# Performance work log

Hardware: AMD Instinct MI355X
Metric: run time of the kernel (lower is better)

Reference implementation:

```python
import jax, jax.numpy as jnp
import numpy as np

NC = 5          # tess_size: number of cells on [0,1]
EPS = 1e-10
BIG = 1e10      # stand-in for 'never hits boundary'


def _make_basis(nC):
    # Continuity constraints of the piecewise-affine velocity v(x)=a_c x + b_c
    # at interior knots x_k = k/nC; basis = null space of L via SVD (basis='svd').
    L = np.zeros((nC - 1, 2 * nC), dtype=np.float64)
    for k in range(1, nC):
        xk = k / nC
        i = k - 1
        L[i, 2 * i: 2 * i + 2] = [xk, 1.0]
        L[i, 2 * (i + 1): 2 * (i + 1) + 2] = [-xk, -1.0]
    _, _, Vt = np.linalg.svd(L)
    return np.ascontiguousarray(Vt[nC - 1:].T).astype(np.float32)  # (2nC, nC+1)

_B = _make_basis(NC)


def _cpab_transform(x, A):
    """Closed-form integration of the CPA ODE x' = a_c x + b_c for unit time.
    x: (N,) points in [0,1]; A: (nC,2) per-cell (slope, offset).
    Returns (phi(x), dphi/dx). dphi/dx = exp(sum_c a_c * time_in_cell_c).
    Boundary cells extend to +/- inf (zero_boundary=False)."""
    nC = NC
    t_rem = jnp.ones_like(x)
    logjac = jnp.zeros_like(x)
    done = jnp.zeros(x.shape, dtype=bool)
    for _ in range(nC + 1):  # at most nC-1 cell crossings possible
        c = jnp.clip(jnp.floor(x * nC).astype(jnp.int32), 0, nC - 1)
        ac = A[c, 0]
        bc = A[c, 1]
        v = ac * x + bc
        pos = v >= 0
        xb = jnp.where(pos, c + 1, c).astype(x.dtype) / nC   # target boundary
        at_edge = jnp.where(pos, c == nC - 1, c == 0)        # boundary cell: no exit
        vb = ac * xb + bc
        v_safe = jnp.where(jnp.abs(v) > EPS, v, 1.0)
        a_safe = jnp.where(jnp.abs(ac) > EPS, ac, 1.0)
        ratio = vb / v_safe
        # time to hit boundary: log(v(xb)/v(x))/a  (or linear if a==0)
        t_hit = jnp.where(jnp.abs(ac) > EPS,
                          jnp.log(jnp.where(ratio > EPS, ratio, 1.0)) / a_safe,
                          (xb - x) / v_safe)
        valid = (jnp.abs(v) > EPS) & (ratio > EPS) & (~at_edge)
        t_hit = jnp.where(valid, t_hit, BIG)
        cross = (t_hit < t_rem) & (~done)
        t_step = jnp.where(done, 0.0, jnp.where(cross, t_hit, t_rem))
        # in-cell flow: x + v * expm1(a t)/a  (-> x + v t as a -> 0)
        e = jnp.expm1(ac * t_step)
        x_flow = jnp.where(jnp.abs(ac) > EPS, x + v * e / a_safe, x + v * t_step)
        x = jnp.where(done, x, jnp.where(cross, xb, x_flow))
        logjac = logjac + ac * t_step
        t_rem = t_rem - t_step
        done = done | (~cross)
    return x, jnp.exp(logjac)


def setup_inputs() -> dict:
    key = jax.random.key(0)
    k1, k2 = jax.random.split(key)
    N = 4_194_304
    x = jax.random.uniform(k1, (N,), dtype=jnp.float32)
    theta = jax.random.normal(k2, (NC + 1,), dtype=jnp.float32)
    return {
        "x": x,
        "theta": theta,
        "aff_a": jnp.ones((1,), jnp.float32),
        "aff_b": jnp.zeros((1,), jnp.float32),
        "aff_c": jnp.ones((1,), jnp.float32),
        "aff_d": jnp.zeros((1,), jnp.float32),
    }


def reference(x, theta, aff_a, aff_b, aff_c, aff_d):
    B = jnp.asarray(_B)                      # (2nC, d)
    A = (B @ theta).reshape(NC, 2)           # per-cell (slope, offset)
    y = aff_a * x + aff_b
    w, dw_dy = _cpab_transform(y, A)         # T.transform_grid / T.gradient_space
    z = aff_c * w + aff_d
    dz_dx = aff_c * dw_dy * aff_a
    return z, jnp.log(dz_dx)
```

## Files before the change

kernel.cpp:

```cpp
#include <hip/hip_runtime.h>
#include <math.h>

#define NC 5
#define NBASIS (NC + 1)
#define EPSF 1e-10f
#define BIGF 1e10f

typedef float v4f __attribute__((ext_vector_type(4)));

struct BMat { float b[2 * NC][NBASIS]; };

static BMat compute_basis() {
    const int m = NC - 1;
    const int n = 2 * NC;
    double A[NC - 1][2 * NC];
    for (int r = 0; r < m; ++r)
        for (int c = 0; c < n; ++c) A[r][c] = 0.0;
    for (int k = 1; k < NC; ++k) {
        double xk = (double)k / (double)NC;
        int i = k - 1;
        A[i][2 * i]     = xk;   A[i][2 * i + 1] = 1.0;
        A[i][2 * i + 2] = -xk;  A[i][2 * i + 3] = -1.0;
    }
    double tau[NC - 1];
    for (int i = 0; i < m; ++i) {
        double alpha = A[i][i];
        double xs = 0.0;
        for (int j = i + 1; j < n; ++j) xs += A[i][j] * A[i][j];
        double xnorm = sqrt(xs);
        if (xnorm == 0.0) { tau[i] = 0.0; continue; }
        double beta = (alpha >= 0.0 ? -1.0 : 1.0) * sqrt(alpha * alpha + xs);
        tau[i] = (beta - alpha) / beta;
        double inv = 1.0 / (alpha - beta);
        for (int j = i + 1; j < n; ++j) A[i][j] *= inv;
        A[i][i] = beta;
        for (int r = i + 1; r < m; ++r) {
            double dot = A[r][i];
            for (int j = i + 1; j < n; ++j) dot += A[r][j] * A[i][j];
            dot *= tau[i];
            A[r][i] -= dot;
            for (int j = i + 1; j < n; ++j) A[r][j] -= dot * A[i][j];
        }
    }
    BMat B;
    for (int c = 0; c < NBASIS; ++c) {
        double v[2 * NC];
        for (int r = 0; r < n; ++r) v[r] = 0.0;
        v[m + c] = 1.0;
        for (int i = m - 1; i >= 0; --i) {
            double dot = v[i];
            for (int j = i + 1; j < n; ++j) dot += A[i][j] * v[j];
            dot *= tau[i];
            v[i] -= dot;
            for (int j = i + 1; j < n; ++j) v[j] -= dot * A[i][j];
        }
        for (int r = 0; r < n; ++r) B.b[r][c] = (float)v[r];
    }
    return B;
}

__device__ __forceinline__ void classify_pt(
    float ym, int c, float a, float b, float kL, float kR,
    float vL, float vR, const float* tR, int& kind, int& jf)
{
#pragma clang fp contract(off)
    float v = a * ym + b;
    bool pos = (v >= 0.0f);
    float xb = pos ? kR : kL;
    bool at_edge = pos ? (c == NC - 1) : (c == 0);
    float vb = pos ? vR : vL;
    bool vok = fabsf(v) > EPSF;
    float vs = vok ? v : 1.0f;
    float ratio = vb / vs;
    bool aok = fabsf(a) > EPSF;
    float as = aok ? a : 1.0f;
    float t0 = aok ? (logf(ratio > EPSF ? ratio : 1.0f) / as)
                   : ((xb - ym) / vs);
    bool valid = vok && (ratio > EPSF) && (!at_edge);
    if (!valid) t0 = BIGF;
    if (!(t0 < 1.0f)) { kind = 0; jf = c; return; }
    if (!pos)         { kind = 1; jf = c; return; }
    kind = 2;
    int j = c + 1; float T = t0;
    while (j < NC - 1 && (T + tR[j] < 1.0f)) { T += tR[j]; ++j; }
    jf = j;
}

__global__ __launch_bounds__(256) void cpab_fused(
    const float* __restrict__ x, const float* __restrict__ theta,
    const float* __restrict__ pa, const float* __restrict__ pb,
    const float* __restrict__ pc, const float* __restrict__ pd,
    float* __restrict__ out, int N, BMat Bm)
{
#pragma clang fp contract(off)
    __shared__ float sA[2 * NC];
    __shared__ float sa[NC], sb[NC], svL[NC], svR[NC], stR[NC], sljR[NC];
    __shared__ float4 sThr[NC];
    __shared__ float4 sS[NC * 5];
    __shared__ float4 sD[NC * 5];
    __shared__ float sAff[4];
    int tid = threadIdx.x;

    if (tid < 2 * NC) {
        float acc = 0.0f;
#pragma unroll
        for (int j = 0; j < NBASIS; ++j) acc += Bm.b[tid][j] * theta[j];
        sA[tid] = acc;
    }
    if (tid == 2 * NC) {
        sAff[0] = pa[0]; sAff[1] = pb[0]; sAff[2] = pc[0]; sAff[3] = pd[0];
    }
    __syncthreads();

    if (tid < NC) {
        int m = tid;
        float a = sA[2 * m], b = sA[2 * m + 1];
        float kL = (float)m / 5.0f, kR = (float)(m + 1) / 5.0f;
        float vL = a * kL + b, vR = a * kR + b;
        bool vok = fabsf(vL) > EPSF;
        float vs = vok ? vL : 1.0f;
        float ratio = vR / vs;
        bool aok = fabsf(a) > EPSF;
        float as = aok ? a : 1.0f;
        float t = aok ? (logf(ratio > EPSF ? ratio : 1.0f) / as)
                      : ((kR - kL) / vs);
        bool valid = vok && (ratio > EPSF) && (m != NC - 1) && (vL >= 0.0f);
        sa[m] = a; sb[m] = b; svL[m] = vL; svR[m] = vR;
        stR[m]  = valid ? t : BIGF;
        sljR[m] = valid ? (a * t) : 0.0f;
    }
    __syncthreads();

    if (tid < NC) {
        int c = tid;
        float a = sa[c], b = sb[c];
        float kL = (float)c / 5.0f, kR = (float)(c + 1) / 5.0f;
        float vL = svL[c], vR = svR[c];
        bool aok = fabsf(a) > EPSF;
        float cand[4];
        int ncand = 0;
        if (aok) {
            if (c > 0 && vL < -EPSF) cand[ncand++] = (vL * expf(-a) - b) / a;
            float sum = 0.0f;
            for (int j = c; j <= NC - 2; ++j) {
                if (j > c) {
                    if (stR[j] >= 0.5f * BIGF) break;
                    sum += stR[j];
                    if (sum >= 1.0f) break;
                }
                float tau = 1.0f - sum;
                if (ncand < 4) cand[ncand++] = (vR * expf(-a * tau) - b) / a;
            }
        } else {
            if (c > 0 && b < -EPSF) cand[ncand++] = kL - b;
            if (b > EPSF) {
                float sum = 0.0f;
                for (int j = c; j <= NC - 2; ++j) {
                    if (j > c) {
                        if (stR[j] >= 0.5f * BIGF) break;
                        sum += stR[j];
                        if (sum >= 1.0f) break;
                    }
                    float tau = 1.0f - sum;
                    if (ncand < 4) cand[ncand++] = kR - b * tau;
                }
            }
        }
        for (int i = ncand; i < 4; ++i) cand[i] = 1e30f;
        for (int i = 1; i < 4; ++i) {
            float key = cand[i]; int j = i - 1;
            while (j >= 0 && cand[j] > key) { cand[j + 1] = cand[j]; --j; }
            cand[j + 1] = key;
        }
        sThr[c] = make_float4(cand[0], cand[1], cand[2], cand[3]);

        float affa = sAff[0], affb = sAff[1], affc = sAff[2], affd = sAff[3];
        float ljadd = logf(affa * affc);
        (void)affb;
        float aeC = aok ? a : 1e-7f;
        float La  = logf(fabsf(aeC));
        float y0  = -b / aeC;
        for (int g = 0; g < 5; ++g) {
            float lo = (g == 0) ? -1e30f : cand[g - 1];
            float hi = (g == 4) ?  1e30f : cand[g];
            float lo2 = fmaxf(lo, kL), hi2 = fminf(hi, kR);
            float S0 = 0, S1 = 0, S2 = 0, S3 = 0, S4 = 0, D0 = 0, D1 = 0;
            if (lo2 < hi2) {
                float ym = 0.5f * (lo2 + hi2);
                int kind, jf;
                classify_pt(ym, c, a, b, kL, kR, vL, vR, stR, kind, jf);
                if (kind == 0) {
                    float G = aok ? (expm1f(a) / a) : 1.0f;
                    S0 = b * G; S1 = 1.0f + a * G;
                    D0 = a;
                } else if (kind == 1) {
                    S0 = kL;
                    D0 = logf(fabsf(vL)) - La; D1 = -1.0f;
                } else {
                    float PTd = 0.0f, PLd = 0.0f;
                    for (int m2 = c + 1; m2 < jf; ++m2) { PTd += stR[m2]; PLd += sljR[m2]; }
                    float aj  = sa[jf];
                    float aeJ = (fabsf(aj) > EPSF) ? aj : 1e-7f;
                    float Q   = svL[jf] / aeJ;
                    float LVR = logf(vR);
                    S3 = aeJ / aeC;
                    S4 = S3 * (La - LVR) - aeJ * PTd;
                    S2 = Q * expf(aeJ);
                    S0 = (float)jf / 5.0f - Q;
                    D1 = S3 - 1.0f;
                    D0 = (1.0f - S3) * LVR + PLd + aj * (1.0f - PTd) + (S3 - 1.0f) * La;
                }
            }
            int s = c * 5 + g;
            sS[s] = make_float4(affc * S0 + affd, affc * S1, affc * S2, S3);
            sD[s] = make_float4(S4, D0 + ljadd, D1, y0);
        }
    }
    __syncthreads();

    float affa = sAff[0], affb = sAff[1];
    int nv = N >> 2;
    int base = blockIdx.x * 512 + tid;
    const float4* x4 = (const float4*)x;
    v4f* oz = (v4f*)out;
    v4f* ol = (v4f*)(out + N);

    bool ok0 = base < nv;
    bool ok1 = (base + 256) < nv;
    float4 xv0, xv1;
    if (ok0) xv0 = x4[base];
    if (ok1) xv1 = x4[base + 256];

    float xin[8];
    xin[0] = xv0.x; xin[1] = xv0.y; xin[2] = xv0.z; xin[3] = xv0.w;
    xin[4] = xv1.x; xin[5] = xv1.y; xin[6] = xv1.z; xin[7] = xv1.w;
    float zi[8], li[8];
#pragma unroll
    for (int q = 0; q < 8; ++q) {
        float y = affa * xin[q] + affb;
        int c = (int)floorf(y * 5.0f);
        c = c < 0 ? 0 : (c > 4 ? 4 : c);
        float4 th = sThr[c];
        int cnt = (y > th.x) + (y > th.y) + (y > th.z) + (y > th.w);
        int s = c * 5 + cnt;
        float4 S = sS[s];
        float4 D = sD[s];
        float L = __logf(fmaxf(fabsf(y - D.w), 1e-37f));
        float E = __expf(fmaf(S.w, L, D.x));
        zi[q] = fmaf(S.z, E, fmaf(S.y, y, S.x));
        li[q] = fmaf(D.z, L, D.y);
    }
    if (ok0) {
        v4f z0 = {zi[0], zi[1], zi[2], zi[3]};
        v4f l0 = {li[0], li[1], li[2], li[3]};
        __builtin_nontemporal_store(z0, &oz[base]);
        __builtin_nontemporal_store(l0, &ol[base]);
    }
    if (ok1) {
        v4f z1 = {zi[4], zi[5], zi[6], zi[7]};
        v4f l1 = {li[4], li[5], li[6], li[7]};
        __builtin_nontemporal_store(z1, &oz[base + 256]);
        __builtin_nontemporal_store(l1, &ol[base + 256]);
    }
}

extern "C" void kernel_launch(void* const* d_in, const int* in_sizes, int n_in,
                              void* d_out, int out_size, void* d_ws, size_t ws_size,
                              hipStream_t stream) {
    const float* x     = (const float*)d_in[0];
    const float* theta = (const float*)d_in[1];
    const float* pa    = (const float*)d_in[2];
    const float* pb    = (const float*)d_in[3];
    const float* pc    = (const float*)d_in[4];
    const float* pd    = (const float*)d_in[5];
    float* out = (float*)d_out;
    int N = in_sizes[0];

    BMat Bm = compute_basis();

    int nv = N >> 2;
    int grid = (nv + 511) / 512;
    cpab_fused<<<grid, 256, 0, stream>>>(x, theta, pa, pb, pc, pd, out, N, Bm);
}
```

Measured before the change: 16.21 us.

## Replace per-cell threshold table with direct closed-form hit-time evaluation per point

Drops the per-block sorted-threshold and 25-entry segment table setup, which ran serially on a few threads with loops, transcendental calls and an insertion sort. Each point now computes its cell hit time from a log and picks the final cell with prefix sums of crossing times, then evaluates the flow in closed form. The input load is also moved ahead of the coefficient setup so global memory latency overlaps the serial prologue. The trade is more ALU work per element, including an extra exp and branches, and possible numerical differences from the cubic expm1 approximation near zero.

```diff
diff --git a/kernel.cpp b/kernel.cpp
--- a/kernel.cpp
+++ b/kernel.cpp
@@ -59,33 +59,6 @@
     return B;
 }
 
-__device__ __forceinline__ void classify_pt(
-    float ym, int c, float a, float b, float kL, float kR,
-    float vL, float vR, const float* tR, int& kind, int& jf)
-{
-#pragma clang fp contract(off)
-    float v = a * ym + b;
-    bool pos = (v >= 0.0f);
-    float xb = pos ? kR : kL;
-    bool at_edge = pos ? (c == NC - 1) : (c == 0);
-    float vb = pos ? vR : vL;
-    bool vok = fabsf(v) > EPSF;
-    float vs = vok ? v : 1.0f;
-    float ratio = vb / vs;
-    bool aok = fabsf(a) > EPSF;
-    float as = aok ? a : 1.0f;
-    float t0 = aok ? (logf(ratio > EPSF ? ratio : 1.0f) / as)
-                   : ((xb - ym) / vs);
-    bool valid = vok && (ratio > EPSF) && (!at_edge);
-    if (!valid) t0 = BIGF;
-    if (!(t0 < 1.0f)) { kind = 0; jf = c; return; }
-    if (!pos)         { kind = 1; jf = c; return; }
-    kind = 2;
-    int j = c + 1; float T = t0;
-    while (j < NC - 1 && (T + tR[j] < 1.0f)) { T += tR[j]; ++j; }
-    jf = j;
-}
-
 __global__ __launch_bounds__(256) void cpab_fused(
     const float* __restrict__ x, const float* __restrict__ theta,
     const float* __restrict__ pa, const float* __restrict__ pb,
@@ -94,12 +67,22 @@
 {
 #pragma clang fp contract(off)
     __shared__ float sA[2 * NC];
-    __shared__ float sa[NC], sb[NC], svL[NC], svR[NC], stR[NC], sljR[NC];
-    __shared__ float4 sThr[NC];
-    __shared__ float4 sS[NC * 5];
-    __shared__ float4 sD[NC * 5];
+    __shared__ float sa[NC], sb[NC], stR[NC], sljR[NC];
+    __shared__ float4 sC1[NC];
+    __shared__ float4 sC2[NC];
+    __shared__ float4 sC3[NC];
+    __shared__ float sFu[3];
     __shared__ float sAff[4];
     int tid = threadIdx.x;
+
+    int nv = N >> 2;
+    int base = blockIdx.x * 512 + tid;
+    bool ok0 = base < nv;
+    bool ok1 = (base + 256) < nv;
+    float4 xv0, xv1;
+    const float4* x4 = (const float4*)x;
+    if (ok0) xv0 = x4[base];
+    if (ok1) xv1 = x4[base + 256];
 
     if (tid < 2 * NC) {
         float acc = 0.0f;
@@ -125,7 +108,7 @@
         float t = aok ? (logf(ratio > EPSF ? ratio : 1.0f) / as)
                       : ((kR - kL) / vs);
         bool valid = vok && (ratio > EPSF) && (m != NC - 1) && (vL >= 0.0f);
-        sa[m] = a; sb[m] = b; svL[m] = vL; svR[m] = vR;
+        sa[m] = a; sb[m] = b;
         stR[m]  = valid ? t : BIGF;
         sljR[m] = valid ? (a * t) : 0.0f;
     }
@@ -134,102 +117,37 @@
     if (tid < NC) {
         int c = tid;
         float a = sa[c], b = sb[c];
-        float kL = (float)c / 5.0f, kR = (float)(c + 1) / 5.0f;
-        float vL = svL[c], vR = svR[c];
         bool aok = fabsf(a) > EPSF;
-        float cand[4];
-        int ncand = 0;
-        if (aok) {
-            if (c > 0 && vL < -EPSF) cand[ncand++] = (vL * expf(-a) - b) / a;
-            float sum = 0.0f;
-            for (int j = c; j <= NC - 2; ++j) {
-                if (j > c) {
-                    if (stR[j] >= 0.5f * BIGF) break;
-                    sum += stR[j];
-                    if (sum >= 1.0f) break;
-                }
-                float tau = 1.0f - sum;
-                if (ncand < 4) cand[ncand++] = (vR * expf(-a * tau) - b) / a;
-            }
-        } else {
-            if (c > 0 && b < -EPSF) cand[ncand++] = kL - b;
-            if (b > EPSF) {
-                float sum = 0.0f;
-                for (int j = c; j <= NC - 2; ++j) {
-                    if (j > c) {
-                        if (stR[j] >= 0.5f * BIGF) break;
-                        sum += stR[j];
-                        if (sum >= 1.0f) break;
-                    }
-                    float tau = 1.0f - sum;
-                    if (ncand < 4) cand[ncand++] = kR - b * tau;
-                }
-            }
+        float ae  = aok ? a : 1e-7f;
+        float rcp = 1.0f / ae;
+        float y0  = -b * rcp;
+        float La  = logf(fabsf(ae));
+        float kLx = (float)c / 5.0f, kRx = (float)(c + 1) / 5.0f;
+        float veL = ae * kLx + b;
+        float veR = ae * kRx + b;
+        float KP1 = (c == NC - 1 || veR <= 0.0f)
+                    ? BIGF : (logf(fabsf(veR)) - La) * rcp;
+        float KP2 = (c == 0 || veL >= 0.0f)
+                    ? BIGF : (logf(fabsf(veL)) - La) * rcp;
+        float F[NC + 1], G[NC + 1];
+        F[0] = 0.0f; G[0] = 0.0f;
+#pragma unroll
+        for (int m = 0; m < NC; ++m) {
+            F[m + 1] = F[m] + fminf(stR[m], 2.0f);
+            G[m + 1] = G[m] + ((stR[m] < 2.0f) ? sljR[m] : 0.0f);
         }
-        for (int i = ncand; i < 4; ++i) cand[i] = 1e30f;
-        for (int i = 1; i < 4; ++i) {
-            float key = cand[i]; int j = i - 1;
-            while (j >= 0 && cand[j] > key) { cand[j + 1] = cand[j]; --j; }
-            cand[j + 1] = key;
-        }
-        sThr[c] = make_float4(cand[0], cand[1], cand[2], cand[3]);
-
-        float affa = sAff[0], affb = sAff[1], affc = sAff[2], affd = sAff[3];
-        float ljadd = logf(affa * affc);
-        (void)affb;
-        float aeC = aok ? a : 1e-7f;
-        float La  = logf(fabsf(aeC));
-        float y0  = -b / aeC;
-        for (int g = 0; g < 5; ++g) {
-            float lo = (g == 0) ? -1e30f : cand[g - 1];
-            float hi = (g == 4) ?  1e30f : cand[g];
-            float lo2 = fmaxf(lo, kL), hi2 = fminf(hi, kR);
-            float S0 = 0, S1 = 0, S2 = 0, S3 = 0, S4 = 0, D0 = 0, D1 = 0;
-            if (lo2 < hi2) {
-                float ym = 0.5f * (lo2 + hi2);
-                int kind, jf;
-                classify_pt(ym, c, a, b, kL, kR, vL, vR, stR, kind, jf);
-                if (kind == 0) {
-                    float G = aok ? (expm1f(a) / a) : 1.0f;
-                    S0 = b * G; S1 = 1.0f + a * G;
-                    D0 = a;
-                } else if (kind == 1) {
-                    S0 = kL;
-                    D0 = logf(fabsf(vL)) - La; D1 = -1.0f;
-                } else {
-                    float PTd = 0.0f, PLd = 0.0f;
-                    for (int m2 = c + 1; m2 < jf; ++m2) { PTd += stR[m2]; PLd += sljR[m2]; }
-                    float aj  = sa[jf];
-                    float aeJ = (fabsf(aj) > EPSF) ? aj : 1e-7f;
-                    float Q   = svL[jf] / aeJ;
-                    float LVR = logf(vR);
-                    S3 = aeJ / aeC;
-                    S4 = S3 * (La - LVR) - aeJ * PTd;
-                    S2 = Q * expf(aeJ);
-                    S0 = (float)jf / 5.0f - Q;
-                    D1 = S3 - 1.0f;
-                    D0 = (1.0f - S3) * LVR + PLd + aj * (1.0f - PTd) + (S3 - 1.0f) * La;
-                }
-            }
-            int s = c * 5 + g;
-            sS[s] = make_float4(affc * S0 + affd, affc * S1, affc * S2, S3);
-            sD[s] = make_float4(S4, D0 + ljadd, D1, y0);
-        }
+        sC1[c] = make_float4(y0, rcp, KP1, KP2);
+        sC2[c] = make_float4(expm1f(ae), a, F[c + 1], G[c + 1]);
+        sC3[c] = make_float4(veL * rcp, ae, F[c], G[c]);
+        if (c == 0) { sFu[0] = F[2]; sFu[1] = F[3]; sFu[2] = F[4]; }
     }
     __syncthreads();
 
-    float affa = sAff[0], affb = sAff[1];
-    int nv = N >> 2;
-    int base = blockIdx.x * 512 + tid;
-    const float4* x4 = (const float4*)x;
+    float affa = sAff[0], affb = sAff[1], affc = sAff[2], affd = sAff[3];
+    float ljadd = logf(affa * affc);
+    float vF2 = sFu[0], vF3 = sFu[1], vF4 = sFu[2];
     v4f* oz = (v4f*)out;
     v4f* ol = (v4f*)(out + N);
-
-    bool ok0 = base < nv;
-    bool ok1 = (base + 256) < nv;
-    float4 xv0, xv1;
-    if (ok0) xv0 = x4[base];
-    if (ok1) xv1 = x4[base + 256];
 
     float xin[8];
     xin[0] = xv0.x; xin[1] = xv0.y; xin[2] = xv0.z; xin[3] = xv0.w;
@@ -240,15 +158,35 @@
         float y = affa * xin[q] + affb;
         int c = (int)floorf(y * 5.0f);
         c = c < 0 ? 0 : (c > 4 ? 4 : c);
-        float4 th = sThr[c];
-        int cnt = (y > th.x) + (y > th.y) + (y > th.z) + (y > th.w);
-        int s = c * 5 + cnt;
-        float4 S = sS[s];
-        float4 D = sD[s];
-        float L = __logf(fmaxf(fabsf(y - D.w), 1e-37f));
-        float E = __expf(fmaf(S.w, L, D.x));
-        zi[q] = fmaf(S.z, E, fmaf(S.y, y, S.x));
-        li[q] = fmaf(D.z, L, D.y);
+        float4 C1 = sC1[c];
+        float4 C2 = sC2[c];
+        float d = y - C1.x;
+        float L = __logf(fmaxf(fabsf(d), 1e-37f));
+        float Lr = L * C1.y;
+        bool pos = (d >= 0.0f) == (C1.y > 0.0f);
+        float t = (pos ? C1.z : C1.w) - Lr;
+        bool cross = (t < 1.0f);
+        float ts = cross ? t : 1.0f;
+        float lj_c = C2.y * ts;
+        float znc = fmaf(d, C2.x, y);
+        float R = 1.0f - t + C2.z;
+        int j = c + 1;
+        j += (c <= 0 && vF2 < R) ? 1 : 0;
+        j += (c <= 1 && vF3 < R) ? 1 : 0;
+        j += (c <= 2 && vF4 < R) ? 1 : 0;
+        j = j > 4 ? 4 : j;
+        float4 C3 = sC3[j];
+        float TT = 1.0f - t - (C3.z - C2.z);
+        float arg = C3.y * TT;
+        float E = __expf(arg) - 1.0f;
+        float pm = arg * (1.0f + arg * (0.5f + arg * 0.16666667f));
+        if (fabsf(arg) < 0.03f) E = pm;
+        float zc  = fmaf(C3.x, E, (float)j * 0.2f);
+        float ljx = lj_c + (C3.w - C2.w) + arg;
+        float z  = cross ? (pos ? zc : (float)c * 0.2f) : znc;
+        float lj = (cross && pos) ? ljx : lj_c;
+        zi[q] = fmaf(affc, z, affd);
+        li[q] = lj + ljadd;
     }
     if (ok0) {
         v4f z0 = {zi[0], zi[1], zi[2], zi[3]};
```

After: 16.58 us. +2.3%, slower.
